# Kernel optimization log

Hardware: AMD Instinct MI355X
Metric: run time of the kernel (lower is better)

## Reference

```python
import jax, jax.numpy as jnp
import numpy as np

CODEBOOK_SIZE = 8192
DECAY = 0.99  # codebook_decay


def setup_inputs() -> dict:
    key = jax.random.key(0)
    k1, k2 = jax.random.split(key)
    N, D, K = 32768, 512, CODEBOOK_SIZE
    target = jax.random.normal(k1, (N, D), dtype=jnp.float32)
    codebook = jax.random.normal(k2, (K, D), dtype=jnp.float32)
    counts = jnp.ones((K,), dtype=jnp.float32)
    return {"target": target, "codebook": codebook, "counts": counts}


def reference(target, codebook, counts):
    # target: [N, D]; codebook: [K, D] (running EMA sum); counts: [K] (running EMA count)
    K = codebook.shape[0]
    cb = codebook / counts[:, None]  # normalized code vectors, [K, D]

    # cdist(target, cb, p=2).argmin(1): argmin of squared euclidean distance
    # ||t - c||^2 = ||t||^2 - 2 t.c + ||c||^2   (||t||^2 constant over codes)
    d2 = (
        jnp.sum(target * target, axis=1, keepdims=True)  # [N, 1]
        - 2.0 * target @ cb.T                             # [N, K]
        + jnp.sum(cb * cb, axis=1)[None, :]               # [1, K]
    )
    labels = jnp.argmin(d2, axis=1)                       # [N]
    onehot = jax.nn.one_hot(labels, K, dtype=jnp.float32)  # [N, K]

    # EMA step (training path): per-code histogram + per-code sum of targets
    count = jax.ops.segment_sum(jnp.ones_like(labels, dtype=jnp.float32), labels, num_segments=K)  # [K]
    memory = jax.ops.segment_sum(target, labels, num_segments=K)  # [K, D] == onehot.T @ target

    alpha = jnp.where(count != 0, DECAY, 1.0)             # [K]
    new_counts = alpha * counts + (1.0 - alpha) * count
    new_codebook = alpha[:, None] * codebook + (1.0 - alpha)[:, None] * memory
    return onehot, new_codebook, new_counts
```

## Files before the change

kernel.cpp:

```cpp
#include <hip/hip_runtime.h>
#include <hip/hip_fp16.h>

typedef _Float16 f16;
typedef _Float16 f16x8 __attribute__((ext_vector_type(8)));
typedef _Float16 f16x4 __attribute__((ext_vector_type(4)));
typedef float    f32x4 __attribute__((ext_vector_type(4)));

#define DECAY   0.99f
#define MARGIN  0.3f
#define MARGIN2 2e-3f
#define MAXA    4096

#define BM    128
#define CT    128
#define BD    64
#define NSPAN 2
#define NSPAN2 32

__device__ __forceinline__ void gl_lds16(const void* g, void* l) {
  __builtin_amdgcn_global_load_lds(
      (const __attribute__((address_space(1))) unsigned int*)g,
      (__attribute__((address_space(3))) unsigned int*)l, 16, 0, 0);
}

__global__ void prep_cb(const float* __restrict__ codebook, const float* __restrict__ counts,
                        f16* __restrict__ cHi, f16* __restrict__ cLo, float* __restrict__ cnorm,
                        unsigned* __restrict__ hist, unsigned* __restrict__ cnts, int D) {
  const int k = blockIdx.x;
  const int tid = threadIdx.x;
  const float cnt = counts[k];
  float4 v = ((const float4*)(codebook + (size_t)k * D))[tid];
  float c0 = v.x / cnt, c1 = v.y / cnt, c2 = v.z / cnt, c3 = v.w / cnt;
  f16 h0 = (f16)c0, h1 = (f16)c1, h2 = (f16)c2, h3 = (f16)c3;
  f16x4 h = {h0, h1, h2, h3};
  f16x4 l = {(f16)(c0 - (float)h0), (f16)(c1 - (float)h1),
             (f16)(c2 - (float)h2), (f16)(c3 - (float)h3)};
  *(f16x4*)(cHi + (size_t)k * D + tid * 4) = h;
  *(f16x4*)(cLo + (size_t)k * D + tid * 4) = l;
  float s = c0*c0 + c1*c1 + c2*c2 + c3*c3;
  #pragma unroll
  for (int m = 1; m < 64; m <<= 1) s += __shfl_xor(s, m);
  __shared__ float red[2];
  if ((tid & 63) == 0) red[tid >> 6] = s;
  __syncthreads();
  if (tid == 0) {
    cnorm[k] = red[0] + red[1];
    hist[k] = 0u;
    if (k == 0) { cnts[0] = 0u; cnts[64] = 0u; }
  }
}

__global__ void prep_t(const float4* __restrict__ t4, f16x4* __restrict__ hi4, long total4) {
  for (long i = blockIdx.x * (long)blockDim.x + threadIdx.x; i < total4;
       i += (long)gridDim.x * blockDim.x) {
    float4 v = t4[i];
    f16x4 h = {(f16)v.x, (f16)v.y, (f16)v.z, (f16)v.w};
    hi4[i] = h;
  }
}

__global__ __launch_bounds__(256, 2)
void argmin_pass(const f16* __restrict__ tHi, const f16* __restrict__ cHi,
                 const float* __restrict__ cnorm, float4* __restrict__ partials,
                 int D, int CSPAN) {
  __shared__ __align__(16) unsigned char smem[5 * 16384];
  unsigned char* ldsA = smem;
  unsigned char* ldsB = smem + 32768;
  float* ldsCn = (float*)(smem + 65536);

  const int tid = threadIdx.x;
  const int w = tid >> 6, lane = tid & 63;
  const int rowBase = blockIdx.x * BM;
  const int colBase = blockIdx.y * CSPAN;

  int rloc[4], exel[4], ldsOff[4];
  #pragma unroll
  for (int i = 0; i < 4; ++i) {
    int s = (i * 4 + w) * 64 + lane;
    int r = s >> 3, c = s & 7;
    rloc[i] = r;
    exel[i] = (c ^ (r & 7)) * 8;
    ldsOff[i] = (i * 4 + w) * 1024;
  }
  size_t aBase[4];
  #pragma unroll
  for (int i = 0; i < 4; ++i) aBase[i] = (size_t)(rowBase + rloc[i]) * D + exel[i];

  const int DS = D / BD;
  const int NT = CSPAN / CT;

  #pragma unroll
  for (int i = 0; i < 4; ++i)
    gl_lds16(cnorm + colBase + (i * 4 + w) * 256 + lane * 4, (unsigned char*)ldsCn + ldsOff[i]);
  #pragma unroll
  for (int i = 0; i < 4; ++i)
    gl_lds16(tHi + aBase[i], ldsA + ldsOff[i]);
  #pragma unroll
  for (int i = 0; i < 4; ++i)
    gl_lds16(cHi + (size_t)(colBase + rloc[i]) * D + exel[i], ldsB + ldsOff[i]);

  float rm1[8], rm2[8];
  unsigned ra1[8];
  #pragma unroll
  for (int i = 0; i < 8; ++i) { rm1[i] = __builtin_inff(); rm2[i] = __builtin_inff(); ra1[i] = 0u; }

  int buf = 0;
  #pragma unroll 1
  for (int tile = 0; tile < NT; ++tile) {
    const int c0 = colBase + tile * CT;

    f32x4 acc[2][8];
    #pragma unroll
    for (int m = 0; m < 2; ++m)
      #pragma unroll
      for (int n = 0; n < 8; ++n) { f32x4 z = {0.f, 0.f, 0.f, 0.f}; acc[m][n] = z; }

    #pragma unroll 1
    for (int ds = 0; ds < DS; ++ds) {
      int dsN = ds + 1, tileN = tile;
      if (dsN == DS) { dsN = 0; tileN = (tile + 1 == NT) ? 0 : tile + 1; }
      const int d0N = dsN * BD;
      const size_t bRow = (size_t)(colBase + tileN * CT);
      unsigned char* lAn = ldsA + ((buf ^ 1) << 14);
      unsigned char* lBn = ldsB + ((buf ^ 1) << 14);
      #pragma unroll
      for (int i = 0; i < 4; ++i)
        gl_lds16(tHi + aBase[i] + d0N, lAn + ldsOff[i]);
      #pragma unroll
      for (int i = 0; i < 4; ++i)
        gl_lds16(cHi + (bRow + rloc[i]) * D + exel[i] + d0N, lBn + ldsOff[i]);

      asm volatile("s_waitcnt vmcnt(8)" ::: "memory");
      __builtin_amdgcn_s_barrier();

      unsigned char* lA = ldsA + (buf << 14);
      unsigned char* lB = ldsB + (buf << 14);
      __builtin_amdgcn_s_setprio(1);
      #pragma unroll
      for (int ks = 0; ks < 2; ++ks) {
        const int chunk = ks * 4 + (lane >> 4);
        f16x8 af[2];
        #pragma unroll
        for (int m = 0; m < 2; ++m) {
          int r = w * 32 + m * 16 + (lane & 15);
          af[m] = *(const f16x8*)(lA + r * 128 + ((chunk ^ (r & 7)) * 16));
        }
        f16x8 bfr[8];
        #pragma unroll
        for (int n = 0; n < 8; ++n) {
          int r = n * 16 + (lane & 15);
          bfr[n] = *(const f16x8*)(lB + r * 128 + ((chunk ^ (r & 7)) * 16));
        }
        #pragma unroll
        for (int m = 0; m < 2; ++m)
          #pragma unroll
          for (int n = 0; n < 8; ++n)
            acc[m][n] = __builtin_amdgcn_mfma_f32_16x16x32_f16(af[m], bfr[n], acc[m][n], 0, 0, 0);
      }
      __builtin_amdgcn_s_setprio(0);

      if (ds == DS - 1) {
        float cn[8];
        #pragma unroll
        for (int n = 0; n < 8; ++n) cn[n] = ldsCn[(tile << 7) + n * 16 + (lane & 15)];
        #pragma unroll
        for (int m = 0; m < 2; ++m) {
          #pragma unroll
          for (int j = 0; j < 4; ++j) {
            float m1 = __builtin_inff(), m2 = __builtin_inff();
            unsigned a1 = 0u;
            #pragma unroll
            for (int n = 0; n < 8; ++n) {
              float v = fmaf(-2.0f, acc[m][n][j], cn[n]);
              unsigned c = (unsigned)(c0 + n * 16 + (lane & 15));
              if (v < m1) { m2 = m1; m1 = v; a1 = c; }
              else if (v < m2) { m2 = v; }
            }
            #pragma unroll
            for (int msk = 1; msk < 16; msk <<= 1) {
              float o1 = __shfl_xor(m1, msk);
              unsigned oa = (unsigned)__shfl_xor((int)a1, msk);
              float o2 = __shfl_xor(m2, msk);
              bool bet = (o1 < m1) || (o1 == m1 && oa < a1);
              float nm2 = bet ? fminf(m1, o2) : fminf(m2, o1);
              if (bet) { m1 = o1; a1 = oa; }
              m2 = nm2;
            }
            const int idx = m * 4 + j;
            bool bet = (m1 < rm1[idx]) || (m1 == rm1[idx] && a1 < ra1[idx]);
            float nm2 = bet ? fminf(rm1[idx], m2) : fminf(rm2[idx], m1);
            if (bet) { rm1[idx] = m1; ra1[idx] = a1; }
            rm2[idx] = nm2;
          }
        }
      }

      asm volatile("s_waitcnt lgkmcnt(0)" ::: "memory");
      __builtin_amdgcn_s_barrier();
      buf ^= 1;
    }
  }

  if ((lane & 15) == 0) {
    const int g = lane >> 4;
    #pragma unroll
    for (int m = 0; m < 2; ++m)
      #pragma unroll
      for (int j = 0; j < 4; ++j) {
        int r = rowBase + w * 32 + m * 16 + g * 4 + j;
        const int idx = m * 4 + j;
        float4 p;
        p.x = rm1[idx];
        p.y = __uint_as_float(ra1[idx]);
        p.z = rm2[idx];
        p.w = 0.f;
        partials[(size_t)r * NSPAN + blockIdx.y] = p;
      }
  }
}

__global__ void reduce_labels(const float4* __restrict__ partials, int* __restrict__ labels,
                              unsigned* __restrict__ cnts, unsigned* __restrict__ list1,
                              unsigned* __restrict__ list2, int N) {
  int r = blockIdx.x * blockDim.x + threadIdx.x;
  if (r >= N) return;
  float m1 = __builtin_inff(), m2 = __builtin_inff();
  unsigned a1 = 0u;
  #pragma unroll
  for (int s = 0; s < NSPAN; ++s) {
    float4 p = partials[(size_t)r * NSPAN + s];
    float o1 = p.x;
    unsigned oa = __float_as_uint(p.y);
    float o2 = p.z;
    bool bet = (o1 < m1) || (o1 == m1 && oa < a1);
    float nm2 = bet ? fminf(m1, o2) : fminf(m2, o1);
    if (bet) { m1 = o1; a1 = oa; }
    m2 = nm2;
  }
  labels[r] = (int)a1;
  if (m2 - m1 < MARGIN) {
    unsigned idx = atomicAdd(&cnts[0], 1u);
    if (idx < MAXA) list1[idx] = (unsigned)r;
    else { unsigned i2 = atomicAdd(&cnts[64], 1u); list2[i2] = (unsigned)r; }
  }
}

__global__ void gather_k(const float4* __restrict__ t4, const unsigned* __restrict__ cnts,
                         const unsigned* __restrict__ list1, f16x4* __restrict__ gHi4,
                         f16x4* __restrict__ gLo4) {
  unsigned i = blockIdx.x * blockDim.x + threadIdx.x;
  unsigned a = i >> 7, j = i & 127;
  unsigned cntA = cnts[0] < MAXA ? cnts[0] : MAXA;
  if (a >= cntA) return;
  unsigned r = list1[a];
  float4 v = t4[(size_t)r * 128 + j];
  f16 h0 = (f16)v.x, h1 = (f16)v.y, h2 = (f16)v.z, h3 = (f16)v.w;
  f16x4 h = {h0, h1, h2, h3};
  f16x4 l = {(f16)(v.x - (float)h0), (f16)(v.y - (float)h1),
             (f16)(v.z - (float)h2), (f16)(v.w - (float)h3)};
  gHi4[(size_t)a * 128 + j] = h;
  gLo4[(size_t)a * 128 + j] = l;
}

__global__ __launch_bounds__(256, 2)
void refine_mfma(const f16* __restrict__ gHi, const f16* __restrict__ gLo,
                 const f16* __restrict__ cHi, const f16* __restrict__ cLo,
                 const float* __restrict__ cnorm, const unsigned* __restrict__ cnts,
                 float4* __restrict__ partials2, int D) {
  __shared__ __align__(16) unsigned char smem[2 * BM * BD * 2];
  unsigned char* ldsA = smem;
  unsigned char* ldsB = smem + BM * BD * 2;

  const unsigned cntA = cnts[0] < MAXA ? cnts[0] : MAXA;
  const int rowBase = blockIdx.x * BM;
  if ((unsigned)rowBase >= cntA) return;
  const int colBase = blockIdx.y * 256;

  const int tid = threadIdx.x;
  const int w = tid >> 6, lane = tid & 63;

  int rloc[4], exel[4], ldsOff[4];
  #pragma unroll
  for (int i = 0; i < 4; ++i) {
    int s = (i * 4 + w) * 64 + lane;
    int r = s >> 3, c = s & 7;
    rloc[i] = r;
    exel[i] = (c ^ (r & 7)) * 8;
    ldsOff[i] = (i * 4 + w) * 1024;
  }
  size_t aBase[4];
  #pragma unroll
  for (int i = 0; i < 4; ++i) aBase[i] = (size_t)(rowBase + rloc[i]) * D + exel[i];

  float rm1[8], rm2[8];
  unsigned ra1[8];
  #pragma unroll
  for (int i = 0; i < 8; ++i) { rm1[i] = __builtin_inff(); rm2[i] = __builtin_inff(); ra1[i] = 0u; }

  #pragma unroll 1
  for (int tile = 0; tile < 2; ++tile) {
    const int c0 = colBase + tile * CT;
    size_t bOff[4];
    #pragma unroll
    for (int i = 0; i < 4; ++i) bOff[i] = (size_t)(c0 + rloc[i]) * D + exel[i];

    f32x4 acc[2][8];
    #pragma unroll
    for (int m = 0; m < 2; ++m)
      #pragma unroll
      for (int n = 0; n < 8; ++n) { f32x4 z = {0.f, 0.f, 0.f, 0.f}; acc[m][n] = z; }

    #pragma unroll 1
    for (int pass = 0; pass < 3; ++pass) {
      const f16* __restrict__ A = (pass == 2) ? gLo : gHi;
      const f16* __restrict__ B = (pass == 1) ? cLo : cHi;
      #pragma unroll 1
      for (int ds = 0; ds < 8; ++ds) {
        const int d0 = ds * BD;
        __syncthreads();
        #pragma unroll
        for (int i = 0; i < 4; ++i) gl_lds16(A + aBase[i] + d0, ldsA + ldsOff[i]);
        #pragma unroll
        for (int i = 0; i < 4; ++i) gl_lds16(B + bOff[i] + d0, ldsB + ldsOff[i]);
        __syncthreads();
        #pragma unroll
        for (int ks = 0; ks < 2; ++ks) {
          const int chunk = ks * 4 + (lane >> 4);
          f16x8 af[2];
          #pragma unroll
          for (int m = 0; m < 2; ++m) {
            int r = w * 32 + m * 16 + (lane & 15);
            af[m] = *(const f16x8*)(ldsA + r * 128 + ((chunk ^ (r & 7)) * 16));
          }
          f16x8 bfr[8];
          #pragma unroll
          for (int n = 0; n < 8; ++n) {
            int r = n * 16 + (lane & 15);
            bfr[n] = *(const f16x8*)(ldsB + r * 128 + ((chunk ^ (r & 7)) * 16));
          }
          #pragma unroll
          for (int m = 0; m < 2; ++m)
            #pragma unroll
            for (int n = 0; n < 8; ++n)
              acc[m][n] = __builtin_amdgcn_mfma_f32_16x16x32_f16(af[m], bfr[n], acc[m][n], 0, 0, 0);
        }
      }
    }

    float cn[8];
    #pragma unroll
    for (int n = 0; n < 8; ++n) cn[n] = cnorm[c0 + n * 16 + (lane & 15)];
    #pragma unroll
    for (int m = 0; m < 2; ++m) {
      #pragma unroll
      for (int j = 0; j < 4; ++j) {
        float m1 = __builtin_inff(), m2 = __builtin_inff();
        unsigned a1 = 0u;
        #pragma unroll
        for (int n = 0; n < 8; ++n) {
          float v = fmaf(-2.0f, acc[m][n][j], cn[n]);
          unsigned c = (unsigned)(c0 + n * 16 + (lane & 15));
          if (v < m1) { m2 = m1; m1 = v; a1 = c; }
          else if (v < m2) { m2 = v; }
        }
        #pragma unroll
        for (int msk = 1; msk < 16; msk <<= 1) {
          float o1 = __shfl_xor(m1, msk);
          unsigned oa = (unsigned)__shfl_xor((int)a1, msk);
          float o2 = __shfl_xor(m2, msk);
          bool bet = (o1 < m1) || (o1 == m1 && oa < a1);
          float nm2 = bet ? fminf(m1, o2) : fminf(m2, o1);
          if (bet) { m1 = o1; a1 = oa; }
          m2 = nm2;
        }
        const int idx = m * 4 + j;
        bool bet = (m1 < rm1[idx]) || (m1 == rm1[idx] && a1 < ra1[idx]);
        float nm2 = bet ? fminf(rm1[idx], m2) : fminf(rm2[idx], m1);
        if (bet) { rm1[idx] = m1; ra1[idx] = a1; }
        rm2[idx] = nm2;
      }
    }
  }

  if ((lane & 15) == 0) {
    const int g = lane >> 4;
    #pragma unroll
    for (int m = 0; m < 2; ++m)
      #pragma unroll
      for (int j = 0; j < 4; ++j) {
        int a = rowBase + w * 32 + m * 16 + g * 4 + j;
        const int idx = m * 4 + j;
        float4 p;
        p.x = rm1[idx];
        p.y = __uint_as_float(ra1[idx]);
        p.z = rm2[idx];
        p.w = 0.f;
        partials2[(size_t)a * NSPAN2 + blockIdx.y] = p;
      }
  }
}

__global__ void reduce2(const float4* __restrict__ partials2, const unsigned* __restrict__ list1,
                        unsigned* __restrict__ cnts, unsigned* __restrict__ list2,
                        int* __restrict__ labels) {
  unsigned a = blockIdx.x * blockDim.x + threadIdx.x;
  unsigned cntA = cnts[0] < MAXA ? cnts[0] : MAXA;
  if (a >= cntA) return;
  float m1 = __builtin_inff(), m2 = __builtin_inff();
  unsigned a1 = 0u;
  #pragma unroll 4
  for (int s = 0; s < NSPAN2; ++s) {
    float4 p = partials2[(size_t)a * NSPAN2 + s];
    float o1 = p.x;
    unsigned oa = __float_as_uint(p.y);
    float o2 = p.z;
    bool bet = (o1 < m1) || (o1 == m1 && oa < a1);
    float nm2 = bet ? fminf(m1, o2) : fminf(m2, o1);
    if (bet) { m1 = o1; a1 = oa; }
    m2 = nm2;
  }
  unsigned r = list1[a];
  labels[r] = (int)a1;
  if (m2 - m1 < MARGIN2) {
    unsigned i2 = atomicAdd(&cnts[64], 1u);
    list2[i2] = r;
  }
}

__global__ __launch_bounds__(256)
void refine_scan(const float* __restrict__ target, const float* __restrict__ codebook,
                 const float* __restrict__ counts, const unsigned* __restrict__ cnts,
                 const unsigned* __restrict__ list2,
                 double* __restrict__ pv, int* __restrict__ pi, int K, int D) {
  const unsigned cnt = cnts[64];
  const unsigned nItems = cnt * 8u;
  const int w = threadIdx.x >> 6, lane = threadIdx.x & 63;
  __shared__ double sv[4];
  __shared__ int si[4];
  for (unsigned item = blockIdx.x; item < nItems; item += gridDim.x) {
    const unsigned a = item >> 3;
    const int chunk = (int)(item & 7u);
    const int r = (int)list2[a];
    const float4* t4 = (const float4*)(target + (size_t)r * D);
    float4 ta = t4[lane * 2], tb = t4[lane * 2 + 1];
    double t0 = ta.x, t1 = ta.y, t2 = ta.z, t3 = ta.w;
    double t4v = tb.x, t5 = tb.y, t6 = tb.z, t7 = tb.w;

    double bv = 1e300;
    int bc = 0;
    const int cBase = chunk * (K / 8) + w * (K / 32);
    #pragma unroll 2
    for (int i = 0; i < K / 32; ++i) {
      const int c = cBase + i;
      const float4* cb4 = (const float4*)(codebook + (size_t)c * D);
      float4 ca = cb4[lane * 2], cb = cb4[lane * 2 + 1];
      const double inv = 1.0 / (double)counts[c];
      double s = 0.0, e;
      e = t0 - (double)ca.x * inv; s = fma(e, e, s);
      e = t1 - (double)ca.y * inv; s = fma(e, e, s);
      e = t2 - (double)ca.z * inv; s = fma(e, e, s);
      e = t3 - (double)ca.w * inv; s = fma(e, e, s);
      e = t4v - (double)cb.x * inv; s = fma(e, e, s);
      e = t5 - (double)cb.y * inv; s = fma(e, e, s);
      e = t6 - (double)cb.z * inv; s = fma(e, e, s);
      e = t7 - (double)cb.w * inv; s = fma(e, e, s);
      #pragma unroll
      for (int m = 1; m < 64; m <<= 1) s += __shfl_xor(s, m);
      if (s < bv) { bv = s; bc = c; }
    }
    if (lane == 0) { sv[w] = bv; si[w] = bc; }
    __syncthreads();
    if (threadIdx.x == 0) {
      double m = sv[0];
      int bi = si[0];
      #pragma unroll
      for (int t = 1; t < 4; ++t)
        if (sv[t] < m || (sv[t] == m && si[t] < bi)) { m = sv[t]; bi = si[t]; }
      pv[(size_t)a * 8 + chunk] = m;
      pi[(size_t)a * 8 + chunk] = bi;
    }
    __syncthreads();
  }
}

__global__ void refine_merge(const double* __restrict__ pv, const int* __restrict__ pi,
                             const unsigned* __restrict__ cnts,
                             const unsigned* __restrict__ list2, int* __restrict__ labels) {
  unsigned a = blockIdx.x * blockDim.x + threadIdx.x;
  if (a >= cnts[64]) return;
  double m = pv[(size_t)a * 8];
  int best = pi[(size_t)a * 8];
  #pragma unroll
  for (int c = 1; c < 8; ++c) {
    double v = pv[(size_t)a * 8 + c];
    int idx = pi[(size_t)a * 8 + c];
    if (v < m || (v == m && idx < best)) { m = v; best = idx; }
  }
  labels[list2[a]] = best;
}

__global__ void hist_k(const int* __restrict__ labels, unsigned* __restrict__ hist, int N) {
  int n = blockIdx.x * blockDim.x + threadIdx.x;
  if (n < N) atomicAdd(&hist[labels[n]], 1u);
}

__global__ void counts_k(const float* __restrict__ counts, const unsigned* __restrict__ hist,
                         float* __restrict__ outCnt, int K) {
  int k = blockIdx.x * blockDim.x + threadIdx.x;
  if (k >= K) return;
  unsigned h = hist[k];
  float alpha = h ? DECAY : 1.0f;
  outCnt[k] = alpha * counts[k] + (1.0f - alpha) * (float)h;
}

__global__ void init_cb(const float4* __restrict__ cb4, const unsigned* __restrict__ hist,
                        float4* __restrict__ out4) {
  int k = blockIdx.x * 2 + (threadIdx.x >> 7);
  int d4 = threadIdx.x & 127;
  float alpha = hist[k] ? DECAY : 1.0f;
  size_t i = (size_t)k * 128 + d4;
  float4 v = cb4[i];
  v.x *= alpha; v.y *= alpha; v.z *= alpha; v.w *= alpha;
  out4[i] = v;
}

__global__ void scatter_k(const float4* __restrict__ t4, const int* __restrict__ labels,
                          float* __restrict__ outCb) {
  int n = blockIdx.x * 2 + (threadIdx.x >> 7);
  int d4 = threadIdx.x & 127;
  int lab = labels[n];
  float4 v = t4[(size_t)n * 128 + d4];
  float* dst = outCb + (size_t)lab * 512 + (d4 << 2);
  const float cc = 1.0f - DECAY;
  atomicAdd(dst + 0, cc * v.x);
  atomicAdd(dst + 1, cc * v.y);
  atomicAdd(dst + 2, cc * v.z);
  atomicAdd(dst + 3, cc * v.w);
}

__global__ void onehot_k(const int* __restrict__ labels, float4* __restrict__ out, int K4) {
  const int n = blockIdx.x;
  const int lab = labels[n];
  const int lab4 = lab >> 2;
  float4* row = out + (size_t)n * K4;
  const float4 z = {0.f, 0.f, 0.f, 0.f};
  for (int c4 = threadIdx.x; c4 < K4; c4 += blockDim.x) {
    if (c4 != lab4) {
      row[c4] = z;
    } else {
      float4 v = z;
      ((float*)&v)[lab & 3] = 1.0f;
      row[c4] = v;
    }
  }
}

extern "C" void kernel_launch(void* const* d_in, const int* in_sizes, int n_in,
                              void* d_out, int out_size, void* d_ws, size_t ws_size,
                              hipStream_t stream) {
  const float* target   = (const float*)d_in[0];
  const float* codebook = (const float*)d_in[1];
  const float* counts   = (const float*)d_in[2];
  const int K = in_sizes[2];
  const int D = in_sizes[1] / K;
  const int N = in_sizes[0] / D;
  const int CSPAN = K / NSPAN;

  float* outOnehot = (float*)d_out;
  float* outCb  = outOnehot + (size_t)N * K;
  float* outCnt = outCb + (size_t)K * D;

  unsigned char* p = (unsigned char*)d_ws;
  f16* tHi = (f16*)p;       p += (size_t)N * D * 2;
  f16* cHi = (f16*)p;       p += (size_t)K * D * 2;
  f16* cLo = (f16*)p;       p += (size_t)K * D * 2;
  float* cnorm = (float*)p; p += (size_t)K * 4;
  float4* partials = (float4*)p; p += (size_t)N * NSPAN * 16;
  int* labels = (int*)p;    p += (size_t)N * 4;
  unsigned* hist = (unsigned*)p;  p += (size_t)K * 4;
  unsigned* cnts = (unsigned*)p;  p += 512;
  unsigned* list1 = (unsigned*)p; p += (size_t)MAXA * 4;
  unsigned* list2 = (unsigned*)p; p += (size_t)N * 4;
  f16* gHi = (f16*)p;       p += (size_t)MAXA * D * 2;
  f16* gLo = (f16*)p;       p += (size_t)MAXA * D * 2;
  float4* partials2 = (float4*)p; p += (size_t)MAXA * NSPAN2 * 16;
  double* refpv = (double*)p;     p += (size_t)N * 8 * 8;
  int* refpi = (int*)p;           p += (size_t)N * 8 * 4;
  if ((size_t)(p - (unsigned char*)d_ws) > ws_size) return;

  hipLaunchKernelGGL(prep_cb, dim3(K), dim3(128), 0, stream,
                     codebook, counts, cHi, cLo, cnorm, hist, cnts, D);
  hipLaunchKernelGGL(prep_t, dim3(2048), dim3(256), 0, stream,
                     (const float4*)target, (f16x4*)tHi, (long)((size_t)N * D / 4));
  hipLaunchKernelGGL(argmin_pass, dim3(N / BM, NSPAN), dim3(256), 0, stream,
                     tHi, cHi, cnorm, partials, D, CSPAN);
  hipLaunchKernelGGL(reduce_labels, dim3((N + 255) / 256), dim3(256), 0, stream,
                     partials, labels, cnts, list1, list2, N);
  hipLaunchKernelGGL(gather_k, dim3(MAXA * 128 / 256), dim3(256), 0, stream,
                     (const float4*)target, cnts, list1, (f16x4*)gHi, (f16x4*)gLo);
  hipLaunchKernelGGL(refine_mfma, dim3(MAXA / BM, NSPAN2), dim3(256), 0, stream,
                     gHi, gLo, cHi, cLo, cnorm, cnts, partials2, D);
  hipLaunchKernelGGL(reduce2, dim3((MAXA + 255) / 256), dim3(256), 0, stream,
                     partials2, list1, cnts, list2, labels);
  hipLaunchKernelGGL(refine_scan, dim3(2048), dim3(256), 0, stream,
                     target, codebook, counts, cnts, list2, refpv, refpi, K, D);
  hipLaunchKernelGGL(refine_merge, dim3((N + 255) / 256), dim3(256), 0, stream,
                     refpv, refpi, cnts, list2, labels);
  hipLaunchKernelGGL(hist_k, dim3((N + 255) / 256), dim3(256), 0, stream, labels, hist, N);
  hipLaunchKernelGGL(counts_k, dim3((K + 255) / 256), dim3(256), 0, stream, counts, hist, outCnt, K);
  hipLaunchKernelGGL(init_cb, dim3(K / 2), dim3(256), 0, stream,
                     (const float4*)codebook, hist, (float4*)outCb);
  hipLaunchKernelGGL(scatter_k, dim3(N / 2), dim3(256), 0, stream,
                     (const float4*)target, labels, outCb);
  hipLaunchKernelGGL(onehot_k, dim3(N), dim3(256), 0, stream,
                     labels, (float4*)outOnehot, K / 4);
}
```

Baseline: 1.249 ms.

## Retile argmin GEMM to 256x256 blocks with per-span partials

```diff
diff --git a/kernel.cpp b/kernel.cpp
--- a/kernel.cpp
+++ b/kernel.cpp
@@ -11,10 +11,10 @@
 #define MARGIN2 2e-3f
 #define MAXA    4096
 
-#define BM    128
-#define CT    128
-#define BD    64
-#define NSPAN 2
+#define BM    256
+#define BN    256
+#define BK    64
+#define NSPANS 128
 #define NSPAN2 32
 
 __device__ __forceinline__ void gl_lds16(const void* g, void* l) {
@@ -59,163 +59,127 @@
   }
 }
 
-__global__ __launch_bounds__(256, 2)
+__global__ __launch_bounds__(512, 2)
 void argmin_pass(const f16* __restrict__ tHi, const f16* __restrict__ cHi,
                  const float* __restrict__ cnorm, float4* __restrict__ partials,
-                 int D, int CSPAN) {
-  __shared__ __align__(16) unsigned char smem[5 * 16384];
+                 int D, int Nrows) {
+  __shared__ __align__(16) unsigned char smem[131072];
   unsigned char* ldsA = smem;
-  unsigned char* ldsB = smem + 32768;
-  float* ldsCn = (float*)(smem + 65536);
+  unsigned char* ldsB = smem + 65536;
 
   const int tid = threadIdx.x;
   const int w = tid >> 6, lane = tid & 63;
+  const int wm = w >> 2, wn = w & 3;
   const int rowBase = blockIdx.x * BM;
-  const int colBase = blockIdx.y * CSPAN;
-
-  int rloc[4], exel[4], ldsOff[4];
+  const int colBase = blockIdx.y * BN;
+
+  int aOff[4], bOff[4];
+  unsigned ldsOff[4];
   #pragma unroll
   for (int i = 0; i < 4; ++i) {
-    int s = (i * 4 + w) * 64 + lane;
+    int s = (i * 8 + w) * 64 + lane;
     int r = s >> 3, c = s & 7;
-    rloc[i] = r;
-    exel[i] = (c ^ (r & 7)) * 8;
-    ldsOff[i] = (i * 4 + w) * 1024;
-  }
-  size_t aBase[4];
-  #pragma unroll
-  for (int i = 0; i < 4; ++i) aBase[i] = (size_t)(rowBase + rloc[i]) * D + exel[i];
-
-  const int DS = D / BD;
-  const int NT = CSPAN / CT;
-
-  #pragma unroll
-  for (int i = 0; i < 4; ++i)
-    gl_lds16(cnorm + colBase + (i * 4 + w) * 256 + lane * 4, (unsigned char*)ldsCn + ldsOff[i]);
-  #pragma unroll
-  for (int i = 0; i < 4; ++i)
-    gl_lds16(tHi + aBase[i], ldsA + ldsOff[i]);
-  #pragma unroll
-  for (int i = 0; i < 4; ++i)
-    gl_lds16(cHi + (size_t)(colBase + rloc[i]) * D + exel[i], ldsB + ldsOff[i]);
-
-  float rm1[8], rm2[8];
-  unsigned ra1[8];
-  #pragma unroll
-  for (int i = 0; i < 8; ++i) { rm1[i] = __builtin_inff(); rm2[i] = __builtin_inff(); ra1[i] = 0u; }
+    int exel = (c ^ (r & 7)) * 8;
+    aOff[i] = (rowBase + r) * D + exel;
+    bOff[i] = (colBase + r) * D + exel;
+    ldsOff[i] = (i * 8 + w) * 1024;
+  }
+
+  f32x4 acc[8][4];
+  #pragma unroll
+  for (int m = 0; m < 8; ++m)
+    #pragma unroll
+    for (int n = 0; n < 4; ++n) { f32x4 z = {0.f, 0.f, 0.f, 0.f}; acc[m][n] = z; }
+
+  #pragma unroll
+  for (int i = 0; i < 4; ++i) gl_lds16(tHi + aOff[i], ldsA + ldsOff[i]);
+  #pragma unroll
+  for (int i = 0; i < 4; ++i) gl_lds16(cHi + bOff[i], ldsB + ldsOff[i]);
 
   int buf = 0;
   #pragma unroll 1
-  for (int tile = 0; tile < NT; ++tile) {
-    const int c0 = colBase + tile * CT;
-
-    f32x4 acc[2][8];
-    #pragma unroll
-    for (int m = 0; m < 2; ++m)
-      #pragma unroll
-      for (int n = 0; n < 8; ++n) { f32x4 z = {0.f, 0.f, 0.f, 0.f}; acc[m][n] = z; }
-
-    #pragma unroll 1
-    for (int ds = 0; ds < DS; ++ds) {
-      int dsN = ds + 1, tileN = tile;
-      if (dsN == DS) { dsN = 0; tileN = (tile + 1 == NT) ? 0 : tile + 1; }
-      const int d0N = dsN * BD;
-      const size_t bRow = (size_t)(colBase + tileN * CT);
-      unsigned char* lAn = ldsA + ((buf ^ 1) << 14);
-      unsigned char* lBn = ldsB + ((buf ^ 1) << 14);
-      #pragma unroll
-      for (int i = 0; i < 4; ++i)
-        gl_lds16(tHi + aBase[i] + d0N, lAn + ldsOff[i]);
-      #pragma unroll
-      for (int i = 0; i < 4; ++i)
-        gl_lds16(cHi + (bRow + rloc[i]) * D + exel[i] + d0N, lBn + ldsOff[i]);
-
-      asm volatile("s_waitcnt vmcnt(8)" ::: "memory");
-      __builtin_amdgcn_s_barrier();
-
-      unsigned char* lA = ldsA + (buf << 14);
-      unsigned char* lB = ldsB + (buf << 14);
-      __builtin_amdgcn_s_setprio(1);
-      #pragma unroll
-      for (int ks = 0; ks < 2; ++ks) {
-        const int chunk = ks * 4 + (lane >> 4);
-        f16x8 af[2];
+  for (int t = 0; t < 8; ++t) {
+    const int d0N = ((t + 1) & 7) * BK;
+    unsigned char* lAn = ldsA + ((buf ^ 1) << 15);
+    unsigned char* lBn = ldsB + ((buf ^ 1) << 15);
+    #pragma unroll
+    for (int i = 0; i < 4; ++i) gl_lds16(tHi + aOff[i] + d0N, lAn + ldsOff[i]);
+    #pragma unroll
+    for (int i = 0; i < 4; ++i) gl_lds16(cHi + bOff[i] + d0N, lBn + ldsOff[i]);
+
+    asm volatile("s_waitcnt vmcnt(8)" ::: "memory");
+    __builtin_amdgcn_s_barrier();
+
+    unsigned char* lA = ldsA + (buf << 15);
+    unsigned char* lB = ldsB + (buf << 15);
+    __builtin_amdgcn_s_setprio(1);
+    #pragma unroll
+    for (int ks = 0; ks < 2; ++ks) {
+      const int chunk = ks * 4 + (lane >> 4);
+      f16x8 af[8];
+      #pragma unroll
+      for (int m = 0; m < 8; ++m) {
+        int r = wm * 128 + m * 16 + (lane & 15);
+        af[m] = *(const f16x8*)(lA + r * 128 + ((chunk ^ (r & 7)) * 16));
+      }
+      f16x8 bfr[4];
+      #pragma unroll
+      for (int n = 0; n < 4; ++n) {
+        int r = wn * 64 + n * 16 + (lane & 15);
+        bfr[n] = *(const f16x8*)(lB + r * 128 + ((chunk ^ (r & 7)) * 16));
+      }
+      #pragma unroll
+      for (int m = 0; m < 8; ++m)
         #pragma unroll
-        for (int m = 0; m < 2; ++m) {
-          int r = w * 32 + m * 16 + (lane & 15);
-          af[m] = *(const f16x8*)(lA + r * 128 + ((chunk ^ (r & 7)) * 16));
-        }
-        f16x8 bfr[8];
-        #pragma unroll
-        for (int n = 0; n < 8; ++n) {
-          int r = n * 16 + (lane & 15);
-          bfr[n] = *(const f16x8*)(lB + r * 128 + ((chunk ^ (r & 7)) * 16));
-        }
-        #pragma unroll
-        for (int m = 0; m < 2; ++m)
-          #pragma unroll
-          for (int n = 0; n < 8; ++n)
-            acc[m][n] = __builtin_amdgcn_mfma_f32_16x16x32_f16(af[m], bfr[n], acc[m][n], 0, 0, 0);
-      }
-      __builtin_amdgcn_s_setprio(0);
-
-      if (ds == DS - 1) {
-        float cn[8];
-        #pragma unroll
-        for (int n = 0; n < 8; ++n) cn[n] = ldsCn[(tile << 7) + n * 16 + (lane & 15)];
-        #pragma unroll
-        for (int m = 0; m < 2; ++m) {
-          #pragma unroll
-          for (int j = 0; j < 4; ++j) {
-            float m1 = __builtin_inff(), m2 = __builtin_inff();
-            unsigned a1 = 0u;
-            #pragma unroll
-            for (int n = 0; n < 8; ++n) {
-              float v = fmaf(-2.0f, acc[m][n][j], cn[n]);
-              unsigned c = (unsigned)(c0 + n * 16 + (lane & 15));
-              if (v < m1) { m2 = m1; m1 = v; a1 = c; }
-              else if (v < m2) { m2 = v; }
-            }
-            #pragma unroll
-            for (int msk = 1; msk < 16; msk <<= 1) {
-              float o1 = __shfl_xor(m1, msk);
-              unsigned oa = (unsigned)__shfl_xor((int)a1, msk);
-              float o2 = __shfl_xor(m2, msk);
-              bool bet = (o1 < m1) || (o1 == m1 && oa < a1);
-              float nm2 = bet ? fminf(m1, o2) : fminf(m2, o1);
-              if (bet) { m1 = o1; a1 = oa; }
-              m2 = nm2;
-            }
-            const int idx = m * 4 + j;
-            bool bet = (m1 < rm1[idx]) || (m1 == rm1[idx] && a1 < ra1[idx]);
-            float nm2 = bet ? fminf(rm1[idx], m2) : fminf(rm2[idx], m1);
-            if (bet) { rm1[idx] = m1; ra1[idx] = a1; }
-            rm2[idx] = nm2;
-          }
-        }
-      }
-
-      asm volatile("s_waitcnt lgkmcnt(0)" ::: "memory");
-      __builtin_amdgcn_s_barrier();
-      buf ^= 1;
-    }
-  }
-
-  if ((lane & 15) == 0) {
-    const int g = lane >> 4;
-    #pragma unroll
-    for (int m = 0; m < 2; ++m)
-      #pragma unroll
-      for (int j = 0; j < 4; ++j) {
-        int r = rowBase + w * 32 + m * 16 + g * 4 + j;
-        const int idx = m * 4 + j;
+        for (int n = 0; n < 4; ++n)
+          acc[m][n] = __builtin_amdgcn_mfma_f32_16x16x32_f16(af[m], bfr[n], acc[m][n], 0, 0, 0);
+    }
+    __builtin_amdgcn_s_setprio(0);
+
+    asm volatile("s_waitcnt lgkmcnt(0)" ::: "memory");
+    __builtin_amdgcn_s_barrier();
+    buf ^= 1;
+  }
+
+  float cn[4];
+  #pragma unroll
+  for (int n = 0; n < 4; ++n) cn[n] = cnorm[colBase + wn * 64 + n * 16 + (lane & 15)];
+
+  const int span = blockIdx.y * 4 + wn;
+  const int g = lane >> 4;
+  #pragma unroll
+  for (int m = 0; m < 8; ++m) {
+    #pragma unroll
+    for (int j = 0; j < 4; ++j) {
+      float m1 = __builtin_inff(), m2 = __builtin_inff();
+      unsigned a1 = 0u;
+      #pragma unroll
+      for (int n = 0; n < 4; ++n) {
+        float v = fmaf(-2.0f, acc[m][n][j], cn[n]);
+        unsigned c = (unsigned)(colBase + wn * 64 + n * 16 + (lane & 15));
+        if (v < m1) { m2 = m1; m1 = v; a1 = c; }
+        else if (v < m2) { m2 = v; }
+      }
+      #pragma unroll
+      for (int msk = 1; msk < 16; msk <<= 1) {
+        float o1 = __shfl_xor(m1, msk);
+        unsigned oa = (unsigned)__shfl_xor((int)a1, msk);
+        float o2 = __shfl_xor(m2, msk);
+        bool bet = (o1 < m1) || (o1 == m1 && oa < a1);
+        float nm2 = bet ? fminf(m1, o2) : fminf(m2, o1);
+        if (bet) { m1 = o1; a1 = oa; }
+        m2 = nm2;
+      }
+      if ((lane & 15) == 0) {
+        int r = rowBase + wm * 128 + m * 16 + g * 4 + j;
         float4 p;
-        p.x = rm1[idx];
-        p.y = __uint_as_float(ra1[idx]);
-        p.z = rm2[idx];
+        p.x = m1;
+        p.y = __uint_as_float(a1);
+        p.z = m2;
         p.w = 0.f;
-        partials[(size_t)r * NSPAN + blockIdx.y] = p;
-      }
+        partials[(size_t)span * Nrows + r] = p;
+      }
+    }
   }
 }
 
@@ -226,9 +190,9 @@
   if (r >= N) return;
   float m1 = __builtin_inff(), m2 = __builtin_inff();
   unsigned a1 = 0u;
-  #pragma unroll
-  for (int s = 0; s < NSPAN; ++s) {
-    float4 p = partials[(size_t)r * NSPAN + s];
+  #pragma unroll 4
+  for (int s = 0; s < NSPANS; ++s) {
+    float4 p = partials[(size_t)s * N + r];
     float o1 = p.x;
     unsigned oa = __float_as_uint(p.y);
     float o2 = p.z;
@@ -267,12 +231,12 @@
                  const f16* __restrict__ cHi, const f16* __restrict__ cLo,
                  const float* __restrict__ cnorm, const unsigned* __restrict__ cnts,
                  float4* __restrict__ partials2, int D) {
-  __shared__ __align__(16) unsigned char smem[2 * BM * BD * 2];
+  __shared__ __align__(16) unsigned char smem[2 * 128 * 64 * 2];
   unsigned char* ldsA = smem;
-  unsigned char* ldsB = smem + BM * BD * 2;
+  unsigned char* ldsB = smem + 128 * 64 * 2;
 
   const unsigned cntA = cnts[0] < MAXA ? cnts[0] : MAXA;
-  const int rowBase = blockIdx.x * BM;
+  const int rowBase = blockIdx.x * 128;
   if ((unsigned)rowBase >= cntA) return;
   const int colBase = blockIdx.y * 256;
 
@@ -299,7 +263,7 @@
 
   #pragma unroll 1
   for (int tile = 0; tile < 2; ++tile) {
-    const int c0 = colBase + tile * CT;
+    const int c0 = colBase + tile * 128;
     size_t bOff[4];
     #pragma unroll
     for (int i = 0; i < 4; ++i) bOff[i] = (size_t)(c0 + rloc[i]) * D + exel[i];
@@ -316,7 +280,7 @@
       const f16* __restrict__ B = (pass == 1) ? cLo : cHi;
       #pragma unroll 1
       for (int ds = 0; ds < 8; ++ds) {
-        const int d0 = ds * BD;
+        const int d0 = ds * 64;
         __syncthreads();
         #pragma unroll
         for (int i = 0; i < 4; ++i) gl_lds16(A + aBase[i] + d0, ldsA + ldsOff[i]);
@@ -564,7 +528,6 @@
   const int K = in_sizes[2];
   const int D = in_sizes[1] / K;
   const int N = in_sizes[0] / D;
-  const int CSPAN = K / NSPAN;
 
   float* outOnehot = (float*)d_out;
   float* outCb  = outOnehot + (size_t)N * K;
@@ -575,7 +538,7 @@
   f16* cHi = (f16*)p;       p += (size_t)K * D * 2;
   f16* cLo = (f16*)p;       p += (size_t)K * D * 2;
   float* cnorm = (float*)p; p += (size_t)K * 4;
-  float4* partials = (float4*)p; p += (size_t)N * NSPAN * 16;
+  float4* partials = (float4*)p; p += (size_t)N * NSPANS * 16;
   int* labels = (int*)p;    p += (size_t)N * 4;
   unsigned* hist = (unsigned*)p;  p += (size_t)K * 4;
   unsigned* cnts = (unsigned*)p;  p += 512;
@@ -592,13 +555,13 @@
                      codebook, counts, cHi, cLo, cnorm, hist, cnts, D);
   hipLaunchKernelGGL(prep_t, dim3(2048), dim3(256), 0, stream,
                      (const float4*)target, (f16x4*)tHi, (long)((size_t)N * D / 4));
-  hipLaunchKernelGGL(argmin_pass, dim3(N / BM, NSPAN), dim3(256), 0, stream,
-                     tHi, cHi, cnorm, partials, D, CSPAN);
+  hipLaunchKernelGGL(argmin_pass, dim3(N / BM, K / BN), dim3(512), 0, stream,
+                     tHi, cHi, cnorm, partials, D, N);
   hipLaunchKernelGGL(reduce_labels, dim3((N + 255) / 256), dim3(256), 0, stream,
                      partials, labels, cnts, list1, list2, N);
   hipLaunchKernelGGL(gather_k, dim3(MAXA * 128 / 256), dim3(256), 0, stream,
                      (const float4*)target, cnts, list1, (f16x4*)gHi, (f16x4*)gLo);
-  hipLaunchKernelGGL(refine_mfma, dim3(MAXA / BM, NSPAN2), dim3(256), 0, stream,
+  hipLaunchKernelGGL(refine_mfma, dim3(MAXA / 128, NSPAN2), dim3(256), 0, stream,
                      gHi, gLo, cHi, cLo, cnorm, cnts, partials2, D);
   hipLaunchKernelGGL(reduce2, dim3((MAXA + 255) / 256), dim3(256), 0, stream,
                      partials2, list1, cnts, list2, labels);
```

Result: slower. 1.318 ms (+5.6%).

## Simplify argmin pass to single-buffered loads and defer cross-lane argmin reduction

Applied to the files above, without the earlier changes.

```diff
diff --git a/kernel.cpp b/kernel.cpp
--- a/kernel.cpp
+++ b/kernel.cpp
@@ -63,10 +63,9 @@
 void argmin_pass(const f16* __restrict__ tHi, const f16* __restrict__ cHi,
                  const float* __restrict__ cnorm, float4* __restrict__ partials,
                  int D, int CSPAN) {
-  __shared__ __align__(16) unsigned char smem[5 * 16384];
+  __shared__ __align__(16) unsigned char smem[2 * BM * BD * 2];
   unsigned char* ldsA = smem;
-  unsigned char* ldsB = smem + 32768;
-  float* ldsCn = (float*)(smem + 65536);
+  unsigned char* ldsB = smem + BM * BD * 2;
 
   const int tid = threadIdx.x;
   const int w = tid >> 6, lane = tid & 63;
@@ -86,28 +85,18 @@
   #pragma unroll
   for (int i = 0; i < 4; ++i) aBase[i] = (size_t)(rowBase + rloc[i]) * D + exel[i];
 
-  const int DS = D / BD;
-  const int NT = CSPAN / CT;
-
-  #pragma unroll
-  for (int i = 0; i < 4; ++i)
-    gl_lds16(cnorm + colBase + (i * 4 + w) * 256 + lane * 4, (unsigned char*)ldsCn + ldsOff[i]);
-  #pragma unroll
-  for (int i = 0; i < 4; ++i)
-    gl_lds16(tHi + aBase[i], ldsA + ldsOff[i]);
-  #pragma unroll
-  for (int i = 0; i < 4; ++i)
-    gl_lds16(cHi + (size_t)(colBase + rloc[i]) * D + exel[i], ldsB + ldsOff[i]);
-
   float rm1[8], rm2[8];
   unsigned ra1[8];
   #pragma unroll
   for (int i = 0; i < 8; ++i) { rm1[i] = __builtin_inff(); rm2[i] = __builtin_inff(); ra1[i] = 0u; }
 
-  int buf = 0;
+  const int NT = CSPAN / CT;
   #pragma unroll 1
   for (int tile = 0; tile < NT; ++tile) {
     const int c0 = colBase + tile * CT;
+    size_t bOff[4];
+    #pragma unroll
+    for (int i = 0; i < 4; ++i) bOff[i] = (size_t)(c0 + rloc[i]) * D + exel[i];
 
     f32x4 acc[2][8];
     #pragma unroll
@@ -116,26 +105,14 @@
       for (int n = 0; n < 8; ++n) { f32x4 z = {0.f, 0.f, 0.f, 0.f}; acc[m][n] = z; }
 
     #pragma unroll 1
-    for (int ds = 0; ds < DS; ++ds) {
-      int dsN = ds + 1, tileN = tile;
-      if (dsN == DS) { dsN = 0; tileN = (tile + 1 == NT) ? 0 : tile + 1; }
-      const int d0N = dsN * BD;
-      const size_t bRow = (size_t)(colBase + tileN * CT);
-      unsigned char* lAn = ldsA + ((buf ^ 1) << 14);
-      unsigned char* lBn = ldsB + ((buf ^ 1) << 14);
-      #pragma unroll
-      for (int i = 0; i < 4; ++i)
-        gl_lds16(tHi + aBase[i] + d0N, lAn + ldsOff[i]);
-      #pragma unroll
-      for (int i = 0; i < 4; ++i)
-        gl_lds16(cHi + (bRow + rloc[i]) * D + exel[i] + d0N, lBn + ldsOff[i]);
-
-      asm volatile("s_waitcnt vmcnt(8)" ::: "memory");
-      __builtin_amdgcn_s_barrier();
-
-      unsigned char* lA = ldsA + (buf << 14);
-      unsigned char* lB = ldsB + (buf << 14);
-      __builtin_amdgcn_s_setprio(1);
+    for (int ds = 0; ds < 8; ++ds) {
+      const int d0 = ds * BD;
+      __syncthreads();
+      #pragma unroll
+      for (int i = 0; i < 4; ++i) gl_lds16(tHi + aBase[i] + d0, ldsA + ldsOff[i]);
+      #pragma unroll
+      for (int i = 0; i < 4; ++i) gl_lds16(cHi + bOff[i] + d0, ldsB + ldsOff[i]);
+      __syncthreads();
       #pragma unroll
       for (int ks = 0; ks < 2; ++ks) {
         const int chunk = ks * 4 + (lane >> 4);
@@ -143,13 +120,13 @@
         #pragma unroll
         for (int m = 0; m < 2; ++m) {
           int r = w * 32 + m * 16 + (lane & 15);
-          af[m] = *(const f16x8*)(lA + r * 128 + ((chunk ^ (r & 7)) * 16));
+          af[m] = *(const f16x8*)(ldsA + r * 128 + ((chunk ^ (r & 7)) * 16));
         }
         f16x8 bfr[8];
         #pragma unroll
         for (int n = 0; n < 8; ++n) {
           int r = n * 16 + (lane & 15);
-          bfr[n] = *(const f16x8*)(lB + r * 128 + ((chunk ^ (r & 7)) * 16));
+          bfr[n] = *(const f16x8*)(ldsB + r * 128 + ((chunk ^ (r & 7)) * 16));
         }
         #pragma unroll
         for (int m = 0; m < 2; ++m)
@@ -157,65 +134,58 @@
           for (int n = 0; n < 8; ++n)
             acc[m][n] = __builtin_amdgcn_mfma_f32_16x16x32_f16(af[m], bfr[n], acc[m][n], 0, 0, 0);
       }
-      __builtin_amdgcn_s_setprio(0);
-
-      if (ds == DS - 1) {
-        float cn[8];
-        #pragma unroll
-        for (int n = 0; n < 8; ++n) cn[n] = ldsCn[(tile << 7) + n * 16 + (lane & 15)];
-        #pragma unroll
-        for (int m = 0; m < 2; ++m) {
-          #pragma unroll
-          for (int j = 0; j < 4; ++j) {
-            float m1 = __builtin_inff(), m2 = __builtin_inff();
-            unsigned a1 = 0u;
-            #pragma unroll
-            for (int n = 0; n < 8; ++n) {
-              float v = fmaf(-2.0f, acc[m][n][j], cn[n]);
-              unsigned c = (unsigned)(c0 + n * 16 + (lane & 15));
-              if (v < m1) { m2 = m1; m1 = v; a1 = c; }
-              else if (v < m2) { m2 = v; }
-            }
-            #pragma unroll
-            for (int msk = 1; msk < 16; msk <<= 1) {
-              float o1 = __shfl_xor(m1, msk);
-              unsigned oa = (unsigned)__shfl_xor((int)a1, msk);
-              float o2 = __shfl_xor(m2, msk);
-              bool bet = (o1 < m1) || (o1 == m1 && oa < a1);
-              float nm2 = bet ? fminf(m1, o2) : fminf(m2, o1);
-              if (bet) { m1 = o1; a1 = oa; }
-              m2 = nm2;
-            }
-            const int idx = m * 4 + j;
-            bool bet = (m1 < rm1[idx]) || (m1 == rm1[idx] && a1 < ra1[idx]);
-            float nm2 = bet ? fminf(rm1[idx], m2) : fminf(rm2[idx], m1);
-            if (bet) { rm1[idx] = m1; ra1[idx] = a1; }
-            rm2[idx] = nm2;
-          }
+    }
+
+    float cn[8];
+    #pragma unroll
+    for (int n = 0; n < 8; ++n) cn[n] = cnorm[c0 + n * 16 + (lane & 15)];
+    #pragma unroll
+    for (int m = 0; m < 2; ++m) {
+      #pragma unroll
+      for (int j = 0; j < 4; ++j) {
+        const int idx = m * 4 + j;
+        float v1 = rm1[idx], v2 = rm2[idx];
+        unsigned b1 = ra1[idx];
+        #pragma unroll
+        for (int n = 0; n < 8; ++n) {
+          float v = fmaf(-2.0f, acc[m][n][j], cn[n]);
+          unsigned c = (unsigned)(c0 + n * 16 + (lane & 15));
+          if (v < v1) { v2 = v1; v1 = v; b1 = c; }
+          else if (v < v2) { v2 = v; }
         }
-      }
-
-      asm volatile("s_waitcnt lgkmcnt(0)" ::: "memory");
-      __builtin_amdgcn_s_barrier();
-      buf ^= 1;
-    }
-  }
-
-  if ((lane & 15) == 0) {
-    const int g = lane >> 4;
-    #pragma unroll
-    for (int m = 0; m < 2; ++m)
-      #pragma unroll
-      for (int j = 0; j < 4; ++j) {
+        rm1[idx] = v1; rm2[idx] = v2; ra1[idx] = b1;
+      }
+    }
+  }
+
+  const int g = lane >> 4;
+  #pragma unroll
+  for (int m = 0; m < 2; ++m) {
+    #pragma unroll
+    for (int j = 0; j < 4; ++j) {
+      const int idx = m * 4 + j;
+      float m1 = rm1[idx], m2 = rm2[idx];
+      unsigned a1 = ra1[idx];
+      #pragma unroll
+      for (int msk = 1; msk < 16; msk <<= 1) {
+        float o1 = __shfl_xor(m1, msk);
+        unsigned oa = (unsigned)__shfl_xor((int)a1, msk);
+        float o2 = __shfl_xor(m2, msk);
+        bool bet = (o1 < m1) || (o1 == m1 && oa < a1);
+        float nm2 = bet ? fminf(m1, o2) : fminf(m2, o1);
+        if (bet) { m1 = o1; a1 = oa; }
+        m2 = nm2;
+      }
+      if ((lane & 15) == 0) {
         int r = rowBase + w * 32 + m * 16 + g * 4 + j;
-        const int idx = m * 4 + j;
         float4 p;
-        p.x = rm1[idx];
-        p.y = __uint_as_float(ra1[idx]);
-        p.z = rm2[idx];
+        p.x = m1;
+        p.y = __uint_as_float(a1);
+        p.z = m2;
         p.w = 0.f;
         partials[(size_t)r * NSPAN + blockIdx.y] = p;
       }
+    }
   }
 }
 
@@ -267,12 +237,12 @@
                  const f16* __restrict__ cHi, const f16* __restrict__ cLo,
                  const float* __restrict__ cnorm, const unsigned* __restrict__ cnts,
                  float4* __restrict__ partials2, int D) {
-  __shared__ __align__(16) unsigned char smem[2 * BM * BD * 2];
+  __shared__ __align__(16) unsigned char smem[2 * 128 * 64 * 2];
   unsigned char* ldsA = smem;
-  unsigned char* ldsB = smem + BM * BD * 2;
+  unsigned char* ldsB = smem + 128 * 64 * 2;
 
   const unsigned cntA = cnts[0] < MAXA ? cnts[0] : MAXA;
-  const int rowBase = blockIdx.x * BM;
+  const int rowBase = blockIdx.x * 128;
   if ((unsigned)rowBase >= cntA) return;
   const int colBase = blockIdx.y * 256;
 
@@ -299,7 +269,7 @@
 
   #pragma unroll 1
   for (int tile = 0; tile < 2; ++tile) {
-    const int c0 = colBase + tile * CT;
+    const int c0 = colBase + tile * 128;
     size_t bOff[4];
     #pragma unroll
     for (int i = 0; i < 4; ++i) bOff[i] = (size_t)(c0 + rloc[i]) * D + exel[i];
@@ -316,7 +286,7 @@
       const f16* __restrict__ B = (pass == 1) ? cLo : cHi;
       #pragma unroll 1
       for (int ds = 0; ds < 8; ++ds) {
-        const int d0 = ds * BD;
+        const int d0 = ds * 64;
         __syncthreads();
         #pragma unroll
         for (int i = 0; i < 4; ++i) gl_lds16(A + aBase[i] + d0, ldsA + ldsOff[i]);
@@ -504,24 +474,18 @@
   if (n < N) atomicAdd(&hist[labels[n]], 1u);
 }
 
-__global__ void counts_k(const float* __restrict__ counts, const unsigned* __restrict__ hist,
-                         float* __restrict__ outCnt, int K) {
-  int k = blockIdx.x * blockDim.x + threadIdx.x;
-  if (k >= K) return;
+__global__ void ema_k(const float4* __restrict__ cb4, const unsigned* __restrict__ hist,
+                      const float* __restrict__ counts, float4* __restrict__ out4,
+                      float* __restrict__ outCnt) {
+  int k = blockIdx.x * 2 + (threadIdx.x >> 7);
+  int d4 = threadIdx.x & 127;
   unsigned h = hist[k];
   float alpha = h ? DECAY : 1.0f;
-  outCnt[k] = alpha * counts[k] + (1.0f - alpha) * (float)h;
-}
-
-__global__ void init_cb(const float4* __restrict__ cb4, const unsigned* __restrict__ hist,
-                        float4* __restrict__ out4) {
-  int k = blockIdx.x * 2 + (threadIdx.x >> 7);
-  int d4 = threadIdx.x & 127;
-  float alpha = hist[k] ? DECAY : 1.0f;
   size_t i = (size_t)k * 128 + d4;
   float4 v = cb4[i];
   v.x *= alpha; v.y *= alpha; v.z *= alpha; v.w *= alpha;
   out4[i] = v;
+  if (d4 == 0) outCnt[k] = alpha * counts[k] + (1.0f - alpha) * (float)h;
 }
 
 __global__ void scatter_k(const float4* __restrict__ t4, const int* __restrict__ labels,
@@ -598,7 +562,7 @@
                      partials, labels, cnts, list1, list2, N);
   hipLaunchKernelGGL(gather_k, dim3(MAXA * 128 / 256), dim3(256), 0, stream,
                      (const float4*)target, cnts, list1, (f16x4*)gHi, (f16x4*)gLo);
-  hipLaunchKernelGGL(refine_mfma, dim3(MAXA / BM, NSPAN2), dim3(256), 0, stream,
+  hipLaunchKernelGGL(refine_mfma, dim3(MAXA / 128, NSPAN2), dim3(256), 0, stream,
                      gHi, gLo, cHi, cLo, cnorm, cnts, partials2, D);
   hipLaunchKernelGGL(reduce2, dim3((MAXA + 255) / 256), dim3(256), 0, stream,
                      partials2, list1, cnts, list2, labels);
@@ -607,9 +571,8 @@
   hipLaunchKernelGGL(refine_merge, dim3((N + 255) / 256), dim3(256), 0, stream,
                      refpv, refpi, cnts, list2, labels);
   hipLaunchKernelGGL(hist_k, dim3((N + 255) / 256), dim3(256), 0, stream, labels, hist, N);
-  hipLaunchKernelGGL(counts_k, dim3((K + 255) / 256), dim3(256), 0, stream, counts, hist, outCnt, K);
-  hipLaunchKernelGGL(init_cb, dim3(K / 2), dim3(256), 0, stream,
-                     (const float4*)codebook, hist, (float4*)outCb);
+  hipLaunchKernelGGL(ema_k, dim3(K / 2), dim3(256), 0, stream,
+                     (const float4*)codebook, hist, counts, (float4*)outCb, outCnt);
   hipLaunchKernelGGL(scatter_k, dim3(N / 2), dim3(256), 0, stream,
                      (const float4*)target, labels, outCb);
   hipLaunchKernelGGL(onehot_k, dim3(N), dim3(256), 0, stream,
```

New measurement: 1.112 ms. -10.9%, faster.
